# Kernel tuning notes

Measured on AMD Instinct MI355X. Metric: run time of the kernel, lower is better.

## Reference

```python
import jax, jax.numpy as jnp
import numpy as np

H = 768
L = 9
M = 5            # max_span_length
CTX_RATIO = 0.5
NEG_INF = -1e30


def setup_inputs() -> dict:
    key = jax.random.key(0)
    ks = jax.random.split(key, 12)
    B, S = 4, 2048
    sc = 1.0 / np.sqrt(H)
    return {
        "sequence_output": jax.random.normal(ks[0], (B, S, H), dtype=jnp.float32),
        "Wc": jax.random.normal(ks[1], (H, L), dtype=jnp.float32) * sc,
        "bc": jnp.zeros((L,), dtype=jnp.float32),
        "wa": jax.random.normal(ks[2], (H,), dtype=jnp.float32) * sc,
        "ba": jnp.zeros((), dtype=jnp.float32),
        "W1": jax.random.normal(ks[3], (2 * H, H), dtype=jnp.float32) * (1.0 / np.sqrt(2 * H)),
        "b1": jnp.zeros((H,), dtype=jnp.float32),
        "gamma": jnp.ones((H,), dtype=jnp.float32),
        "beta": jnp.zeros((H,), dtype=jnp.float32),
        "W2": jax.random.normal(ks[4], (H, L), dtype=jnp.float32) * sc,
        "b2": jnp.zeros((L,), dtype=jnp.float32),
    }


def reference(sequence_output, Wc, bc, wa, ba, W1, b1, gamma, beta, W2, b2):
    x = sequence_output                        # [B,S,H]
    B, S, _ = x.shape
    base_logits = jnp.einsum('bsh,hl->bsl', x, Wc) + bc   # [B,S,L]

    # sliding-window indices: window [i-M, i+M] clipped to [0, S)
    offsets = jnp.arange(-M, M + 1)            # [W]
    idx = jnp.arange(S)[:, None] + offsets     # [S,W]
    valid = (idx >= 0) & (idx < S)             # [S,W]
    idx_c = jnp.clip(idx, 0, S - 1)            # [S,W]

    # attention scores over window (span_attention linear -> scalar per token)
    scores = jnp.einsum('bsh,h->bs', x, wa) + ba           # [B,S]
    win_scores = scores[:, idx_c]                          # [B,S,W]
    win_scores = jnp.where(valid[None], win_scores, NEG_INF)
    attn = jax.nn.softmax(win_scores, axis=-1)             # [B,S,W]

    win_tokens = x[:, idx_c]                               # [B,S,W,H] gather
    weighted_ctx = jnp.einsum('bsw,bswh->bsh', attn, win_tokens)

    token_with_ctx = jnp.concatenate([x, weighted_ctx], axis=-1)  # [B,S,2H]
    h = jnp.einsum('bsd,dh->bsh', token_with_ctx, W1) + b1
    # LayerNorm (eps = 1e-5, torch default)
    mu = jnp.mean(h, axis=-1, keepdims=True)
    var = jnp.mean((h - mu) ** 2, axis=-1, keepdims=True)
    h = (h - mu) * jax.lax.rsqrt(var + 1e-5) * gamma + beta
    h = jax.nn.gelu(h, approximate=False)                  # torch nn.GELU default (erf)
    ctx_logits = jnp.einsum('bsh,hl->bsl', h, W2) + b2

    return (1.0 - CTX_RATIO) * base_logits + CTX_RATIO * ctx_logits
```

## Files before the change

kernel.cpp:

```cpp
#include <hip/hip_runtime.h>
#include <hip/hip_bf16.h>
#include <math.h>

#define S_LEN 2048
#define BATCH 4
#define HDIM 768
#define LOUT 9
#define NROWS (BATCH*S_LEN)
#define K2H 1536
#define WIN 11
#define NEG_INF_F (-1e30f)

typedef __attribute__((ext_vector_type(4))) float f32x4;
typedef __attribute__((ext_vector_type(8))) short bf16x8;

static __device__ __forceinline__ void async_ld16(const void* g, void* l) {
  __builtin_amdgcn_global_load_lds((const __attribute__((address_space(1))) void*)g,
                                   (__attribute__((address_space(3))) void*)l, 16, 0, 0);
}

static __device__ __forceinline__ unsigned short f2bf(float f) {
  union { float f; unsigned int u; } v; v.f = f;
  unsigned int u = v.u;
  unsigned int r = (u + 0x7fffu + ((u >> 16) & 1u)) >> 16;
  return (unsigned short)r;
}

__global__ __launch_bounds__(256) void k_prep_x(const float* __restrict__ x,
                                                unsigned short* __restrict__ xc) {
  int g = blockIdx.x * 256 + threadIdx.x;
  int row = g / 192;
  int c4 = (g % 192) * 4;
  const float4 v = *(const float4*)(x + row * HDIM + c4);
  ushort4 o;
  o.x = f2bf(v.x); o.y = f2bf(v.y); o.z = f2bf(v.z); o.w = f2bf(v.w);
  *(ushort4*)(xc + row * K2H + c4) = o;
}

__global__ __launch_bounds__(256) void k_prep_w1t(const float* __restrict__ W1,
                                                  unsigned short* __restrict__ W1t) {
  __shared__ float tile[32][33];
  int bk = blockIdx.x % 48;
  int bn = blockIdx.x / 48;
  int tc = threadIdx.x % 32;
  int tr = threadIdx.x / 32;
  #pragma unroll
  for (int i = 0; i < 32; i += 8) {
    tile[tr + i][tc] = W1[(bk*32 + tr + i) * HDIM + bn*32 + tc];
  }
  __syncthreads();
  #pragma unroll
  for (int i = 0; i < 32; i += 8) {
    W1t[(bn*32 + tr + i) * K2H + bk*32 + tc] = f2bf(tile[tc][tr + i]);
  }
}

__global__ __launch_bounds__(256) void k_scores(const float* __restrict__ x,
                                                const float* __restrict__ wa,
                                                const float* __restrict__ ba,
                                                float* __restrict__ scores) {
  int wave = threadIdx.x >> 6, lane = threadIdx.x & 63;
  int row = blockIdx.x * 4 + wave;
  const float* xr = x + row * HDIM;
  float acc = 0.f;
  #pragma unroll
  for (int i = 0; i < 12; ++i) acc += xr[i*64 + lane] * wa[i*64 + lane];
  #pragma unroll
  for (int m = 1; m < 64; m <<= 1) acc += __shfl_xor(acc, m);
  if (lane == 0) scores[row] = acc + ba[0];
}

__global__ __launch_bounds__(256) void k_ctx(const float* __restrict__ x,
                                             const float* __restrict__ scores,
                                             const float* __restrict__ Wc,
                                             const float* __restrict__ bc,
                                             unsigned short* __restrict__ xc,
                                             float* __restrict__ base) {
  __shared__ float scl[WIN];
  __shared__ float es[WIN];
  __shared__ int rowidx[WIN];
  __shared__ float red[4][LOUT];
  int row = blockIdx.x;
  int b = row >> 11, s = row & 2047;
  int t = threadIdx.x;
  if (t < WIN) {
    int j = s - 5 + t;
    bool valid = (j >= 0) && (j < S_LEN);
    int jc = valid ? j : (j < 0 ? 0 : S_LEN - 1);
    rowidx[t] = b * S_LEN + jc;
    scl[t] = valid ? scores[b * S_LEN + jc] : NEG_INF_F;
  }
  __syncthreads();
  float mx = scl[0];
  #pragma unroll
  for (int w = 1; w < WIN; ++w) mx = fmaxf(mx, scl[w]);
  if (t < WIN) {
    float sv = scl[t];
    es[t] = (sv > -1e29f) ? __expf(sv - mx) : 0.f;
  }
  __syncthreads();
  float ssum = 0.f;
  #pragma unroll
  for (int w = 0; w < WIN; ++w) ssum += es[w];
  float inv = 1.f / ssum;
  float acc0 = 0.f, acc1 = 0.f, acc2 = 0.f;
  #pragma unroll
  for (int w = 0; w < WIN; ++w) {
    float aw = es[w] * inv;
    const float* xr = x + rowidx[w] * HDIM;
    acc0 += aw * xr[t];
    acc1 += aw * xr[t + 256];
    acc2 += aw * xr[t + 512];
  }
  unsigned short* dst = xc + row * K2H + HDIM;
  dst[t]       = f2bf(acc0);
  dst[t + 256] = f2bf(acc1);
  dst[t + 512] = f2bf(acc2);
  const float* xr = x + row * HDIM;
  float p[LOUT] = {};
  #pragma unroll
  for (int i = 0; i < 3; ++i) {
    int e = t + i * 256;
    float xv = xr[e];
    const float* wrow = Wc + e * LOUT;
    #pragma unroll
    for (int l = 0; l < LOUT; ++l) p[l] += xv * wrow[l];
  }
  #pragma unroll
  for (int l = 0; l < LOUT; ++l) {
    #pragma unroll
    for (int m = 1; m < 64; m <<= 1) p[l] += __shfl_xor(p[l], m);
  }
  int lane = t & 63, wave = t >> 6;
  if (lane == 0) {
    #pragma unroll
    for (int l = 0; l < LOUT; ++l) red[wave][l] = p[l];
  }
  __syncthreads();
  if (t < LOUT) {
    base[row * LOUT + t] = red[0][t] + red[1][t] + red[2][t] + red[3][t] + bc[t];
  }
}

__global__ __launch_bounds__(256) void k_gemm(const unsigned short* __restrict__ A,
                                              const unsigned short* __restrict__ Bt,
                                              const float* __restrict__ b1,
                                              float* __restrict__ Hout) {
  __shared__ unsigned short As[128 * 32];
  __shared__ unsigned short Bs[128 * 32];
  int bid = blockIdx.x;
  int bm = bid / 6, bn = bid % 6;
  int t = threadIdx.x;
  int lane = t & 63, wave = t >> 6;
  int wm = wave >> 1, wn = wave & 1;
  int e0 = t * 8;
  int r0 = e0 >> 5, c0 = e0 & 31;
  const unsigned short* gA0 = A + (bm * 128 + r0) * K2H + c0;
  const unsigned short* gB0 = Bt + (bn * 128 + r0) * K2H + c0;
  unsigned short* lA = As + wave * 512;
  unsigned short* lB = Bs + wave * 512;
  f32x4 acc[4][4] = {};
  int laneRow = lane & 15;
  int laneK = (lane >> 4) * 8;
  const unsigned short* aBase = As + (wm * 64 + laneRow) * 32 + laneK;
  const unsigned short* bBase = Bs + (wn * 64 + laneRow) * 32 + laneK;

  for (int kt = 0; kt < K2H; kt += 32) {
    __syncthreads();
    async_ld16(gA0 + kt, lA);
    async_ld16(gA0 + 64 * K2H + kt, lA + 2048);
    async_ld16(gB0 + kt, lB);
    async_ld16(gB0 + 64 * K2H + kt, lB + 2048);
    __syncthreads();
    bf16x8 a[4], bfr[4];
    #pragma unroll
    for (int m = 0; m < 4; ++m) a[m] = *(const bf16x8*)(aBase + m * 16 * 32);
    #pragma unroll
    for (int n = 0; n < 4; ++n) bfr[n] = *(const bf16x8*)(bBase + n * 16 * 32);
    #pragma unroll
    for (int m = 0; m < 4; ++m)
      #pragma unroll
      for (int n = 0; n < 4; ++n)
        acc[m][n] = __builtin_amdgcn_mfma_f32_16x16x32_bf16(a[m], bfr[n], acc[m][n], 0, 0, 0);
  }
  int orow = bm * 128 + wm * 64 + (lane >> 4) * 4;
  int ocol = bn * 128 + wn * 64 + (lane & 15);
  #pragma unroll
  for (int m = 0; m < 4; ++m)
    #pragma unroll
    for (int n = 0; n < 4; ++n) {
      int col = ocol + n * 16;
      float bv = b1[col];
      #pragma unroll
      for (int r = 0; r < 4; ++r) {
        Hout[(orow + m * 16 + r) * HDIM + col] = acc[m][n][r] + bv;
      }
    }
}

__global__ __launch_bounds__(256) void k_ln(const float* __restrict__ Hin,
                                            const float* __restrict__ gamma,
                                            const float* __restrict__ beta,
                                            const float* __restrict__ W2,
                                            const float* __restrict__ b2,
                                            const float* __restrict__ base,
                                            float* __restrict__ out) {
  __shared__ float redS[4], redQ[4], redp[4][LOUT];
  int row = blockIdx.x;
  int t = threadIdx.x;
  int lane = t & 63, wave = t >> 6;
  const float* hr = Hin + row * HDIM;
  float v0 = hr[t], v1 = hr[t + 256], v2 = hr[t + 512];
  float s1 = v0 + v1 + v2;
  float s2 = v0 * v0 + v1 * v1 + v2 * v2;
  #pragma unroll
  for (int m = 1; m < 64; m <<= 1) { s1 += __shfl_xor(s1, m); s2 += __shfl_xor(s2, m); }
  if (lane == 0) { redS[wave] = s1; redQ[wave] = s2; }
  __syncthreads();
  s1 = redS[0] + redS[1] + redS[2] + redS[3];
  s2 = redQ[0] + redQ[1] + redQ[2] + redQ[3];
  float mu = s1 * (1.f / HDIM);
  float var = s2 * (1.f / HDIM) - mu * mu;
  float rstd = rsqrtf(var + 1e-5f);
  float p[LOUT] = {};
  float vv[3] = { v0, v1, v2 };
  #pragma unroll
  for (int i = 0; i < 3; ++i) {
    int e = t + i * 256;
    float g = (vv[i] - mu) * rstd * gamma[e] + beta[e];
    float gg = 0.5f * g * (1.f + erff(g * 0.70710678118654752f));
    const float* wrow = W2 + e * LOUT;
    #pragma unroll
    for (int l = 0; l < LOUT; ++l) p[l] += gg * wrow[l];
  }
  #pragma unroll
  for (int l = 0; l < LOUT; ++l) {
    #pragma unroll
    for (int m = 1; m < 64; m <<= 1) p[l] += __shfl_xor(p[l], m);
  }
  if (lane == 0) {
    #pragma unroll
    for (int l = 0; l < LOUT; ++l) redp[wave][l] = p[l];
  }
  __syncthreads();
  if (t < LOUT) {
    float cl = redp[0][t] + redp[1][t] + redp[2][t] + redp[3][t] + b2[t];
    out[row * LOUT + t] = 0.5f * base[row * LOUT + t] + 0.5f * cl;
  }
}

extern "C" void kernel_launch(void* const* d_in, const int* in_sizes, int n_in,
                              void* d_out, int out_size, void* d_ws, size_t ws_size,
                              hipStream_t stream) {
  const float* x     = (const float*)d_in[0];
  const float* Wc    = (const float*)d_in[1];
  const float* bc    = (const float*)d_in[2];
  const float* wa    = (const float*)d_in[3];
  const float* ba    = (const float*)d_in[4];
  const float* W1    = (const float*)d_in[5];
  const float* b1    = (const float*)d_in[6];
  const float* gamma = (const float*)d_in[7];
  const float* beta  = (const float*)d_in[8];
  const float* W2    = (const float*)d_in[9];
  const float* b2    = (const float*)d_in[10];
  float* out = (float*)d_out;

  char* ws = (char*)d_ws;
  unsigned short* xc  = (unsigned short*)(ws);
  unsigned short* w1t = (unsigned short*)(ws + 25165824);
  float* scores       = (float*)(ws + 27525120);
  float* base         = (float*)(ws + 27557888);
  float* hbuf         = (float*)(ws + 27852800);

  k_prep_x  <<<dim3(6144), dim3(256), 0, stream>>>(x, xc);
  k_prep_w1t<<<dim3(1152), dim3(256), 0, stream>>>(W1, w1t);
  k_scores  <<<dim3(2048), dim3(256), 0, stream>>>(x, wa, ba, scores);
  k_ctx     <<<dim3(8192), dim3(256), 0, stream>>>(x, scores, Wc, bc, xc, base);
  k_gemm    <<<dim3(384),  dim3(256), 0, stream>>>(xc, w1t, b1, hbuf);
  k_ln      <<<dim3(8192), dim3(256), 0, stream>>>(hbuf, gamma, beta, W2, b2, base, out);
}
```

Measured before the change: 200.0 us.

## Double-buffer GEMM with BK=64 and 128x64 tiles, fuse score into bf16 prep

```diff
diff --git a/kernel.cpp b/kernel.cpp
--- a/kernel.cpp
+++ b/kernel.cpp
@@ -26,15 +26,26 @@
   return (unsigned short)r;
 }
 
-__global__ __launch_bounds__(256) void k_prep_x(const float* __restrict__ x,
-                                                unsigned short* __restrict__ xc) {
-  int g = blockIdx.x * 256 + threadIdx.x;
-  int row = g / 192;
-  int c4 = (g % 192) * 4;
-  const float4 v = *(const float4*)(x + row * HDIM + c4);
+__global__ __launch_bounds__(192) void k_prep(const float* __restrict__ x,
+                                              const float* __restrict__ wa,
+                                              const float* __restrict__ ba,
+                                              unsigned short* __restrict__ xc,
+                                              float* __restrict__ scores) {
+  __shared__ float red[3];
+  int row = blockIdx.x;
+  int t = threadIdx.x;
+  int lane = t & 63, wave = t >> 6;
+  const float4 v = *(const float4*)(x + row * HDIM + t * 4);
+  const float4 w = *(const float4*)(wa + t * 4);
   ushort4 o;
   o.x = f2bf(v.x); o.y = f2bf(v.y); o.z = f2bf(v.z); o.w = f2bf(v.w);
-  *(ushort4*)(xc + row * K2H + c4) = o;
+  *(ushort4*)(xc + row * K2H + t * 4) = o;
+  float p = v.x * w.x + v.y * w.y + v.z * w.z + v.w * w.w;
+  #pragma unroll
+  for (int m = 1; m < 64; m <<= 1) p += __shfl_xor(p, m);
+  if (lane == 0) red[wave] = p;
+  __syncthreads();
+  if (t == 0) scores[row] = red[0] + red[1] + red[2] + ba[0];
 }
 
 __global__ __launch_bounds__(256) void k_prep_w1t(const float* __restrict__ W1,
@@ -53,21 +64,6 @@
   for (int i = 0; i < 32; i += 8) {
     W1t[(bn*32 + tr + i) * K2H + bk*32 + tc] = f2bf(tile[tc][tr + i]);
   }
-}
-
-__global__ __launch_bounds__(256) void k_scores(const float* __restrict__ x,
-                                                const float* __restrict__ wa,
-                                                const float* __restrict__ ba,
-                                                float* __restrict__ scores) {
-  int wave = threadIdx.x >> 6, lane = threadIdx.x & 63;
-  int row = blockIdx.x * 4 + wave;
-  const float* xr = x + row * HDIM;
-  float acc = 0.f;
-  #pragma unroll
-  for (int i = 0; i < 12; ++i) acc += xr[i*64 + lane] * wa[i*64 + lane];
-  #pragma unroll
-  for (int m = 1; m < 64; m <<= 1) acc += __shfl_xor(acc, m);
-  if (lane == 0) scores[row] = acc + ba[0];
 }
 
 __global__ __launch_bounds__(256) void k_ctx(const float* __restrict__ x,
@@ -146,47 +142,69 @@
                                               const unsigned short* __restrict__ Bt,
                                               const float* __restrict__ b1,
                                               float* __restrict__ Hout) {
-  __shared__ unsigned short As[128 * 32];
-  __shared__ unsigned short Bs[128 * 32];
+  __shared__ unsigned short As[2][128 * 64];
+  __shared__ unsigned short Bs[2][64 * 64];
   int bid = blockIdx.x;
-  int bm = bid / 6, bn = bid % 6;
+  int obid = (bid & 7) * 96 + (bid >> 3);
+  int bm = obid / 12, bn = obid % 12;
   int t = threadIdx.x;
   int lane = t & 63, wave = t >> 6;
-  int wm = wave >> 1, wn = wave & 1;
-  int e0 = t * 8;
-  int r0 = e0 >> 5, c0 = e0 & 31;
-  const unsigned short* gA0 = A + (bm * 128 + r0) * K2H + c0;
-  const unsigned short* gB0 = Bt + (bn * 128 + r0) * K2H + c0;
-  unsigned short* lA = As + wave * 512;
-  unsigned short* lB = Bs + wave * 512;
-  f32x4 acc[4][4] = {};
+  int rsub = lane >> 3;
+  int kslot = lane & 7;
+
+  int aRow0 = bm * 128 + (wave * 4 + 0) * 8 + rsub;
+  int bRow0 = bn * 64  + (wave * 2 + 0) * 8 + rsub;
+  const unsigned short* gA = A  + aRow0 * K2H + kslot * 8;
+  const unsigned short* gB = Bt + bRow0 * K2H + kslot * 8;
+
+  f32x4 acc[2][4] = {};
   int laneRow = lane & 15;
   int laneK = (lane >> 4) * 8;
-  const unsigned short* aBase = As + (wm * 64 + laneRow) * 32 + laneK;
-  const unsigned short* bBase = Bs + (wn * 64 + laneRow) * 32 + laneK;
-
-  for (int kt = 0; kt < K2H; kt += 32) {
+  const unsigned short* aBase0 = &As[0][(wave * 32 + laneRow) * 64 + laneK];
+  const unsigned short* bBase0 = &Bs[0][laneRow * 64 + laneK];
+
+#define STAGE(buf, kt) do {                                                   \
+    _Pragma("unroll")                                                         \
+    for (int j = 0; j < 4; ++j)                                               \
+      async_ld16(gA + j * 8 * K2H + (kt), &As[buf][(wave * 4 + j) * 512]);    \
+    _Pragma("unroll")                                                         \
+    for (int j = 0; j < 2; ++j)                                               \
+      async_ld16(gB + j * 8 * K2H + (kt), &Bs[buf][(wave * 2 + j) * 512]);    \
+  } while (0)
+
+#define COMPUTE(buf) do {                                                     \
+    const unsigned short* aB = aBase0 + (buf) * 128 * 64;                     \
+    const unsigned short* bB = bBase0 + (buf) * 64 * 64;                      \
+    _Pragma("unroll")                                                         \
+    for (int kk = 0; kk < 2; ++kk) {                                          \
+      bf16x8 af[2], bf[4];                                                    \
+      _Pragma("unroll")                                                       \
+      for (int m = 0; m < 2; ++m) af[m] = *(const bf16x8*)(aB + m*16*64 + kk*32); \
+      _Pragma("unroll")                                                       \
+      for (int n = 0; n < 4; ++n) bf[n] = *(const bf16x8*)(bB + n*16*64 + kk*32); \
+      _Pragma("unroll")                                                       \
+      for (int m = 0; m < 2; ++m)                                             \
+        _Pragma("unroll")                                                     \
+        for (int n = 0; n < 4; ++n)                                           \
+          acc[m][n] = __builtin_amdgcn_mfma_f32_16x16x32_bf16(af[m], bf[n], acc[m][n], 0, 0, 0); \
+    }                                                                         \
+  } while (0)
+
+  STAGE(0, 0);
+  __syncthreads();
+  int cur = 0;
+  for (int kt = 64; kt < K2H; kt += 64) {
+    STAGE(cur ^ 1, kt);
+    COMPUTE(cur);
     __syncthreads();
-    async_ld16(gA0 + kt, lA);
-    async_ld16(gA0 + 64 * K2H + kt, lA + 2048);
-    async_ld16(gB0 + kt, lB);
-    async_ld16(gB0 + 64 * K2H + kt, lB + 2048);
-    __syncthreads();
-    bf16x8 a[4], bfr[4];
-    #pragma unroll
-    for (int m = 0; m < 4; ++m) a[m] = *(const bf16x8*)(aBase + m * 16 * 32);
-    #pragma unroll
-    for (int n = 0; n < 4; ++n) bfr[n] = *(const bf16x8*)(bBase + n * 16 * 32);
-    #pragma unroll
-    for (int m = 0; m < 4; ++m)
-      #pragma unroll
-      for (int n = 0; n < 4; ++n)
-        acc[m][n] = __builtin_amdgcn_mfma_f32_16x16x32_bf16(a[m], bfr[n], acc[m][n], 0, 0, 0);
-  }
-  int orow = bm * 128 + wm * 64 + (lane >> 4) * 4;
-  int ocol = bn * 128 + wn * 64 + (lane & 15);
-  #pragma unroll
-  for (int m = 0; m < 4; ++m)
+    cur ^= 1;
+  }
+  COMPUTE(cur);
+
+  int orow = bm * 128 + wave * 32 + (lane >> 4) * 4;
+  int ocol = bn * 64 + (lane & 15);
+  #pragma unroll
+  for (int m = 0; m < 2; ++m)
     #pragma unroll
     for (int n = 0; n < 4; ++n) {
       int col = ocol + n * 16;
@@ -196,6 +214,8 @@
         Hout[(orow + m * 16 + r) * HDIM + col] = acc[m][n][r] + bv;
       }
     }
+#undef STAGE
+#undef COMPUTE
 }
 
 __global__ __launch_bounds__(256) void k_ln(const float* __restrict__ Hin,
@@ -272,10 +292,9 @@
   float* base         = (float*)(ws + 27557888);
   float* hbuf         = (float*)(ws + 27852800);
 
-  k_prep_x  <<<dim3(6144), dim3(256), 0, stream>>>(x, xc);
+  k_prep    <<<dim3(8192), dim3(192), 0, stream>>>(x, wa, ba, xc, scores);
   k_prep_w1t<<<dim3(1152), dim3(256), 0, stream>>>(W1, w1t);
-  k_scores  <<<dim3(2048), dim3(256), 0, stream>>>(x, wa, ba, scores);
   k_ctx     <<<dim3(8192), dim3(256), 0, stream>>>(x, scores, Wc, bc, xc, base);
-  k_gemm    <<<dim3(384),  dim3(256), 0, stream>>>(xc, w1t, b1, hbuf);
+  k_gemm    <<<dim3(768),  dim3(256), 0, stream>>>(xc, w1t, b1, hbuf);
   k_ln      <<<dim3(8192), dim3(256), 0, stream>>>(hbuf, gamma, beta, W2, b2, base, out);
 }
```

New measurement: 194.5 us. -2.7%, faster.
